# Kernel tuning notes

Hardware: AMD Instinct MI355X
Metric: run time of the kernel (lower is better)

The kernel has to match this reference:

```python
import jax, jax.numpy as jnp
import numpy as np
from jax import lax

DIM = 128; HEADS = 8; SPLIT = 4; MLP = 4
B = 8; H = 64; W = 64
EPS = 1e-5

def conv1x1(x, w, b):
    # x: (b,c,h,w), w: (o,c), b: (o,)
    return jnp.einsum('oc,bchw->bohw', w, x) + b[None, :, None, None]

def dwconv3(x, w, b):
    # depthwise 3x3, w: (C,1,3,3)
    c = x.shape[1]
    y = lax.conv_general_dilated(x, w, window_strides=(1, 1), padding=((1, 1), (1, 1)),
                                 feature_group_count=c,
                                 dimension_numbers=('NCHW', 'OIHW', 'NCHW'))
    return y + b[None, :, None, None]

def groupnorm1(x, g, bta):
    # GroupNorm with 1 group: normalize over (C,H,W) per sample
    mu = x.mean(axis=(1, 2, 3), keepdims=True)
    var = ((x - mu) ** 2).mean(axis=(1, 2, 3), keepdims=True)
    xn = (x - mu) * lax.rsqrt(var + EPS)
    return xn * g[None, :, None, None] + bta[None, :, None, None]

def eca(x, w):
    b, c, h, w_ = x.shape
    y = x.mean(axis=(2, 3))                         # (b,c)
    y = lax.conv_general_dilated(y[:, None, :], w, window_strides=(1,), padding=((2, 2),),
                                 dimension_numbers=('NCH', 'OIH', 'NCH'))  # (b,1,c)
    gate = jax.nn.sigmoid(y[:, 0])[:, :, None, None]
    return x * gate

def esa(x, alpha):
    x_se = x - x.mean(axis=(2, 3), keepdims=True)   # subtract per-channel GAP
    x_max = x_se.max(axis=1, keepdims=True)
    x_min = x_se.min(axis=1, keepdims=True)
    a = alpha[0]
    return x * jax.nn.sigmoid(x_max) * a + x * jax.nn.sigmoid(x_min) * (1.0 - a)

def eaa(q, k, v, h_sp, w_sp, cpe_w, cpe_b):
    b, c, h, w = q.shape
    hd = c // HEADS
    nh, nw = h // h_sp, w // w_sp
    L = h_sp * w_sp
    cpe = dwconv3(v, cpe_w, cpe_b)
    def win(t):
        t = t.reshape(b, c, nh, h_sp, nw, w_sp)
        t = t.transpose(0, 2, 4, 3, 5, 1).reshape(-1, L, HEADS, hd)
        return t.transpose(0, 2, 1, 3)  # (b*nh*nw, heads, L, hd)
    qw, kw, vw = win(q), win(k), win(v)
    attn = jax.nn.softmax(qw @ kw.transpose(0, 1, 3, 2), axis=-1)  # no scale, as in source
    o = attn @ vw                                    # (b*nh*nw, heads, L, hd)
    o = o.transpose(0, 2, 1, 3).reshape(b, nh, nw, h_sp, w_sp, c)
    o = o.transpose(0, 5, 1, 3, 2, 4).reshape(b, c, h, w)
    return o + cpe

def setup_inputs() -> dict:
    key = jax.random.key(0)
    ks = jax.random.split(key, 16)
    d = DIM
    z = lambda *s: jnp.zeros(s, jnp.float32)
    def n(i, shape, s=0.02):
        return jax.random.normal(ks[i], shape, dtype=jnp.float32) * s
    return dict(
        x=jax.random.normal(ks[0], (B, d, H, W), dtype=jnp.float32),
        eca_w=n(1, (1, 1, 5), 0.2),
        esa_alpha=jnp.ones((1,), jnp.float32),
        cpe1_w=n(2, (d, 1, 3, 3), 0.1), cpe1_b=z(d),
        g1=jnp.ones((d,), jnp.float32), b1=z(d),
        actp_w=n(3, (d, d)), actp_b=z(d),
        inp_w=n(4, (d, d)), inp_b=z(d),
        dwc_w=n(5, (d, 1, 3, 3), 0.1), dwc_b=z(d),
        qkv_w=n(6, (5 * d, d)), qkv_b=z(5 * d),
        eaax_w=n(7, (d, 1, 3, 3), 0.1), eaax_b=z(d),
        eaay_w=n(8, (d, 1, 3, 3), 0.1), eaay_b=z(d),
        outp_w=n(9, (d, d)), outp_b=z(d),
        cpe2_w=n(10, (d, 1, 3, 3), 0.1), cpe2_b=z(d),
        g2=jnp.ones((d,), jnp.float32), b2=z(d),
        mlp1_w=n(11, (MLP * d, d)), mlp1_b=z(MLP * d),
        mlp2_w=n(12, (d, MLP * d)), mlp2_b=z(d),
    )

def reference(x, eca_w, esa_alpha, cpe1_w, cpe1_b, g1, b1, actp_w, actp_b, inp_w, inp_b,
              dwc_w, dwc_b, qkv_w, qkv_b, eaax_w, eaax_b, eaay_w, eaay_b, outp_w, outp_b,
              cpe2_w, cpe2_b, g2, b2, mlp1_w, mlp1_b, mlp2_w, mlp2_b):
    b, c, h, w = x.shape
    x = eca(x, eca_w) + esa(x, esa_alpha)
    x = x + dwconv3(x, cpe1_w, cpe1_b)
    shortcut = x
    xn = groupnorm1(x, g1, b1)
    act_res = jax.nn.relu(conv1x1(xn, actp_w, actp_b))
    t = jax.nn.relu(dwconv3(conv1x1(xn, inp_w, inp_b), dwc_w, dwc_b))
    t = conv1x1(t, qkv_w, qkv_b)                     # (b, 5c, h, w)
    t5 = t.reshape(b, c, 5, h, w)                    # channel i::5 == t5[:,:,i]
    q0, k0, v0, q1, k1 = (t5[:, :, i] for i in range(5))
    a = eaa(q0, k0, v0, h, SPLIT, eaax_w, eaax_b) + eaa(q1, k1, v0, SPLIT, w, eaay_w, eaay_b)
    out = conv1x1(a * act_res, outp_w, outp_b) + shortcut
    out = out + dwconv3(out, cpe2_w, cpe2_b)
    mlp = conv1x1(jax.nn.relu(conv1x1(groupnorm1(out, g2, b2), mlp1_w, mlp1_b)), mlp2_w, mlp2_b)
    return mlp + out
```

## Files before the change

kernel.cpp:

```cpp
#include <hip/hip_runtime.h>

#define NPIX 4096
#define CDIM 128
#define BATCH 8
#define EPSN 1e-5f

typedef __attribute__((ext_vector_type(8))) short short8;
typedef __attribute__((ext_vector_type(4))) float f32x4;
typedef __attribute__((ext_vector_type(16))) float f32x16;

__device__ __forceinline__ float sigmoidf_(float x) { return 1.f / (1.f + __expf(-x)); }

__device__ __forceinline__ unsigned short f2b(float f) {
    unsigned int u = __float_as_uint(f);
    unsigned int r = (u + 0x7FFF + ((u >> 16) & 1)) >> 16;
    return (unsigned short)r;
}
__device__ __forceinline__ float b2f(unsigned short u) {
    return __uint_as_float((unsigned int)u << 16);
}

__device__ __forceinline__ int tok2pix(int mode, int wi, int l) {
    return (mode == 0) ? ((l >> 2) * 64 + wi * 4 + (l & 3))
                       : ((wi * 4 + (l >> 6)) * 64 + (l & 63));
}

__global__ __launch_bounds__(256) void convert_w_kernel(const float* __restrict__ qkv_w,
                                                        const float* __restrict__ mlp1_w,
                                                        const float* __restrict__ mlp2_w,
                                                        const float* __restrict__ actp_w,
                                                        const float* __restrict__ inp_w,
                                                        const float* __restrict__ outp_w,
                                                        const float* __restrict__ qkv_b,
                                                        const float* __restrict__ eaax_w,
                                                        const float* __restrict__ eaax_b,
                                                        const float* __restrict__ eaay_w,
                                                        const float* __restrict__ eaay_b,
                                                        const float* __restrict__ cpe1_w,
                                                        const float* __restrict__ dwc_w,
                                                        const float* __restrict__ cpe2_w,
                                                        unsigned short* __restrict__ dst,
                                                        float* __restrict__ qb_r,
                                                        float* __restrict__ wsT,
                                                        float* __restrict__ bsum,
                                                        float* __restrict__ cpe1T,
                                                        float* __restrict__ dwcT,
                                                        float* __restrict__ cpe2T) {
    int i = blockIdx.x * 256 + threadIdx.x;
    if (i >= 267520) return;
    if (i < 262144) {
        float v;
        if (i < 81920) {
            int o = i >> 7, c = i & 127;
            v = qkv_w[(size_t)(5 * (o & 127) + (o >> 7)) * 128 + c];
        } else if (i < 147456) v = mlp1_w[i - 81920];
        else if (i < 212992)   v = mlp2_w[i - 147456];
        else if (i < 229376)   v = actp_w[i - 212992];
        else if (i < 245760)   v = inp_w[i - 229376];
        else                   v = outp_w[i - 245760];
        dst[i] = f2b(v);
    } else {
        int j = i - 262144;
        if (j < 640) qb_r[j] = qkv_b[5 * (j & 127) + (j >> 7)];
        else if (j < 1792) {
            int idx = j - 640; int k = idx >> 7, c = idx & 127;
            wsT[idx] = eaax_w[c * 9 + k] + eaay_w[c * 9 + k];
        } else if (j < 1920) bsum[j - 1792] = eaax_b[j - 1792] + eaay_b[j - 1792];
        else if (j < 3072) {
            int idx = j - 1920; int k = idx >> 7, c = idx & 127;
            cpe1T[idx] = cpe1_w[c * 9 + k];
        } else if (j < 4224) {
            int idx = j - 3072; int k = idx >> 7, c = idx & 127;
            dwcT[idx] = dwc_w[c * 9 + k];
        } else {
            int idx = j - 4224; int k = idx >> 7, c = idx & 127;
            cpe2T[idx] = cpe2_w[c * 9 + k];
        }
    }
}

__global__ __launch_bounds__(256) void mean_bc_kernel(const float* __restrict__ x,
                                                      float* __restrict__ mean) {
    __shared__ float sb[4];
    int bc = blockIdx.x;
    const float* p = x + (size_t)bc * NPIX;
    float s = 0.f;
    for (int i = threadIdx.x; i < NPIX; i += 256) s += p[i];
#pragma unroll
    for (int off = 32; off > 0; off >>= 1) s += __shfl_down(s, off, 64);
    if ((threadIdx.x & 63) == 0) sb[threadIdx.x >> 6] = s;
    __syncthreads();
    if (threadIdx.x == 0) mean[bc] = (sb[0] + sb[1] + sb[2] + sb[3]) * (1.f / (float)NPIX);
}

__global__ void eca_gate_kernel(const float* __restrict__ mean, const float* __restrict__ w5,
                                float* __restrict__ gate) {
    int b = blockIdx.x, c = threadIdx.x;
    float s = 0.f;
#pragma unroll
    for (int k = 0; k < 5; ++k) {
        int cc = c + k - 2;
        if (cc >= 0 && cc < CDIM) s += w5[k] * mean[b * CDIM + cc];
    }
    gate[b * CDIM + c] = sigmoidf_(s);
}

__global__ __launch_bounds__(256) void esa_tr_kernel(const float* __restrict__ x,
                                                     const float* __restrict__ mean,
                                                     const float* __restrict__ gate,
                                                     const float* __restrict__ alpha_p,
                                                     float* __restrict__ y) {
    __shared__ float tile[128][65];
    __shared__ float smx[4][64], smn[4][64], ssc[64];
    int b = blockIdx.y, p0 = blockIdx.x * 64;
    int tx = threadIdx.x, pl = tx & 63, part = tx >> 6;
    const float* xb = x + (size_t)b * CDIM * NPIX;
    const float* mb = mean + b * CDIM;
    for (int c = part; c < CDIM; c += 4)
        tile[c][pl] = xb[(size_t)c * NPIX + p0 + pl];
    __syncthreads();
    float mx = -1e30f, mn = 1e30f;
#pragma unroll
    for (int cc = 0; cc < 32; ++cc) {
        int c = part * 32 + cc;
        float v = tile[c][pl] - mb[c];
        mx = fmaxf(mx, v); mn = fminf(mn, v);
    }
    smx[part][pl] = mx; smn[part][pl] = mn;
    __syncthreads();
    if (part == 0) {
        float m1 = fmaxf(fmaxf(smx[0][pl], smx[1][pl]), fmaxf(smx[2][pl], smx[3][pl]));
        float m2 = fminf(fminf(smn[0][pl], smn[1][pl]), fminf(smn[2][pl], smn[3][pl]));
        float a = alpha_p[0];
        ssc[pl] = sigmoidf_(m1) * a + sigmoidf_(m2) * (1.f - a);
    }
    __syncthreads();
    const float* gb = gate + b * CDIM;
    int c2 = tx & 127, pr = tx >> 7;
    float* yb = y + ((size_t)b * NPIX + p0) * CDIM;
    float gv = gb[c2];
    for (int p = pr; p < 64; p += 2)
        yb[(size_t)p * CDIM + c2] = tile[c2][p] * (gv + ssc[p]);
}

__global__ __launch_bounds__(256) void cpe_f32_kernel(const float* __restrict__ in,
                                                      const float* __restrict__ wT,
                                                      const float* __restrict__ bias,
                                                      float* __restrict__ out,
                                                      float* __restrict__ stats) {
    __shared__ float sb[8];
    int b = blockIdx.y, tx = threadIdx.x;
    int cg = tx & 15, pp = tx >> 4;
    int p = blockIdx.x * 16 + pp;
    int xx = p & 63, yy = p >> 6;
    int c0 = cg * 8;
    float acc[8], ctr[8];
#pragma unroll
    for (int j = 0; j < 8; ++j) acc[j] = bias[c0 + j];
#pragma unroll
    for (int dy = -1; dy <= 1; ++dy) {
        int y2 = yy + dy;
        if (y2 < 0 || y2 >= 64) continue;
#pragma unroll
        for (int dx = -1; dx <= 1; ++dx) {
            int x2 = xx + dx;
            if (x2 < 0 || x2 >= 64) continue;
            const float* ip = &in[((size_t)b * NPIX + y2 * 64 + x2) * 128 + c0];
            float4 v0 = *(const float4*)ip;
            float4 v1 = *(const float4*)(ip + 4);
            const float* wr = wT + ((dy + 1) * 3 + dx + 1) * 128 + c0;
            acc[0] += v0.x * wr[0]; acc[1] += v0.y * wr[1];
            acc[2] += v0.z * wr[2]; acc[3] += v0.w * wr[3];
            acc[4] += v1.x * wr[4]; acc[5] += v1.y * wr[5];
            acc[6] += v1.z * wr[6]; acc[7] += v1.w * wr[7];
            if (dy == 0 && dx == 0) {
                ctr[0] = v0.x; ctr[1] = v0.y; ctr[2] = v0.z; ctr[3] = v0.w;
                ctr[4] = v1.x; ctr[5] = v1.y; ctr[6] = v1.z; ctr[7] = v1.w;
            }
        }
    }
    float s = 0.f, s2 = 0.f;
    float r[8];
#pragma unroll
    for (int j = 0; j < 8; ++j) {
        r[j] = ctr[j] + acc[j];
        s += r[j]; s2 += r[j] * r[j];
    }
    float* op = &out[((size_t)b * NPIX + p) * 128 + c0];
    *(float4*)op = make_float4(r[0], r[1], r[2], r[3]);
    *(float4*)(op + 4) = make_float4(r[4], r[5], r[6], r[7]);
#pragma unroll
    for (int off = 32; off > 0; off >>= 1) {
        s += __shfl_down(s, off, 64);
        s2 += __shfl_down(s2, off, 64);
    }
    int wv = tx >> 6;
    if ((tx & 63) == 0) { sb[wv] = s; sb[4 + wv] = s2; }
    __syncthreads();
    if (tx == 0) {
        int slot = (b * 8 + (blockIdx.x & 7)) * 16;
        atomicAdd(&stats[slot], sb[0] + sb[1] + sb[2] + sb[3]);
        atomicAdd(&stats[slot + 1], sb[4] + sb[5] + sb[6] + sb[7]);
    }
}

__global__ __launch_bounds__(256) void gn_apply_kernel(const float* __restrict__ in,
                                                       const float* __restrict__ stats,
                                                       const float* __restrict__ g,
                                                       const float* __restrict__ bta,
                                                       unsigned short* __restrict__ dst) {
    int b = blockIdx.y;
    int i = blockIdx.x * 256 + threadIdx.x;
    float su = 0.f, sq = 0.f;
#pragma unroll
    for (int sl = 0; sl < 8; ++sl) {
        su += stats[(b * 8 + sl) * 16];
        sq += stats[(b * 8 + sl) * 16 + 1];
    }
    const float n = 1.f / (float)(CDIM * NPIX);
    float mu = su * n;
    float var = sq * n - mu * mu;
    float rr = rsqrtf(var + EPSN);
    int c0 = (i & 15) * 8;
    size_t idx = (size_t)b * (NPIX * 128) + (size_t)i * 8;
    float4 v0 = *(const float4*)&in[idx];
    float4 v1 = *(const float4*)&in[idx + 4];
    unsigned short o[8];
    o[0] = f2b((v0.x - mu) * rr * g[c0 + 0] + bta[c0 + 0]);
    o[1] = f2b((v0.y - mu) * rr * g[c0 + 1] + bta[c0 + 1]);
    o[2] = f2b((v0.z - mu) * rr * g[c0 + 2] + bta[c0 + 2]);
    o[3] = f2b((v0.w - mu) * rr * g[c0 + 3] + bta[c0 + 3]);
    o[4] = f2b((v1.x - mu) * rr * g[c0 + 4] + bta[c0 + 4]);
    o[5] = f2b((v1.y - mu) * rr * g[c0 + 5] + bta[c0 + 5]);
    o[6] = f2b((v1.z - mu) * rr * g[c0 + 6] + bta[c0 + 6]);
    o[7] = f2b((v1.w - mu) * rr * g[c0 + 7] + bta[c0 + 7]);
    *(uint4*)&dst[idx] = *(uint4*)o;
}

__global__ __launch_bounds__(256) void dwc_bf16_kernel(const unsigned short* __restrict__ in,
                                                       const float* __restrict__ wT,
                                                       const float* __restrict__ bias,
                                                       unsigned short* __restrict__ out) {
    int b = blockIdx.y, tx = threadIdx.x;
    int cg = tx & 15, pp = tx >> 4;
    int p = blockIdx.x * 16 + pp;
    int xx = p & 63, yy = p >> 6;
    int c0 = cg * 8;
    float acc[8];
#pragma unroll
    for (int j = 0; j < 8; ++j) acc[j] = bias[c0 + j];
#pragma unroll
    for (int dy = -1; dy <= 1; ++dy) {
        int y2 = yy + dy;
        if (y2 < 0 || y2 >= 64) continue;
#pragma unroll
        for (int dx = -1; dx <= 1; ++dx) {
            int x2 = xx + dx;
            if (x2 < 0 || x2 >= 64) continue;
            unsigned short v[8];
            *(uint4*)v = *(const uint4*)&in[((size_t)b * NPIX + y2 * 64 + x2) * 128 + c0];
            const float* wr = wT + ((dy + 1) * 3 + dx + 1) * 128 + c0;
#pragma unroll
            for (int j = 0; j < 8; ++j) acc[j] += b2f(v[j]) * wr[j];
        }
    }
    unsigned short o[8];
#pragma unroll
    for (int j = 0; j < 8; ++j) o[j] = f2b(fmaxf(acc[j], 0.f));
    *(uint4*)&out[((size_t)b * NPIX + p) * 128 + c0] = *(uint4*)o;
}

__global__ __launch_bounds__(256) void conv_mfma_kernel(const unsigned short* __restrict__ in_t,
                                                        const unsigned short* __restrict__ w,
                                                        const float* __restrict__ bias,
                                                        const float* __restrict__ res,
                                                        float* __restrict__ out,
                                                        unsigned short* __restrict__ out_t,
                                                        int Cin, int Cout, int relu, int nchw) {
    __shared__ __align__(16) unsigned short A_s[128][136];
    __shared__ __align__(16) unsigned short B_s[128][136];
    int b = blockIdx.z, p0 = blockIdx.x * 128, o0 = blockIdx.y * 128;
    int tx = threadIdx.x;
    int wave = tx >> 6, lane = tx & 63;
    int wm = wave & 1, wn = wave >> 1;
    int quad = lane >> 4, l16 = lane & 15;

    f32x4 acc[4][4];
#pragma unroll
    for (int mt = 0; mt < 4; ++mt) {
#pragma unroll
        for (int r = 0; r < 4; ++r) {
            float bv = bias[o0 + wm * 64 + mt * 16 + quad * 4 + r];
#pragma unroll
            for (int nt = 0; nt < 4; ++nt) acc[mt][nt][r] = bv;
        }
    }

    for (int k0 = 0; k0 < Cin; k0 += 128) {
#pragma unroll
        for (int j = 0; j < 8; ++j) {
            int idx = tx + 256 * j;
            int row = idx >> 4, c16 = idx & 15;
            *(uint4*)&A_s[row][c16 * 8] =
                *(const uint4*)&w[(size_t)(o0 + row) * Cin + k0 + c16 * 8];
            *(uint4*)&B_s[row][c16 * 8] =
                *(const uint4*)&in_t[((size_t)b * NPIX + p0 + row) * Cin + k0 + c16 * 8];
        }
        __syncthreads();
#pragma unroll
        for (int ks = 0; ks < 128; ks += 32) {
            short8 af[4], bf[4];
#pragma unroll
            for (int mt = 0; mt < 4; ++mt)
                af[mt] = *(const short8*)&A_s[wm * 64 + mt * 16 + l16][ks + quad * 8];
#pragma unroll
            for (int nt = 0; nt < 4; ++nt)
                bf[nt] = *(const short8*)&B_s[wn * 64 + nt * 16 + l16][ks + quad * 8];
#pragma unroll
            for (int mt = 0; mt < 4; ++mt)
#pragma unroll
                for (int nt = 0; nt < 4; ++nt)
                    acc[mt][nt] = __builtin_amdgcn_mfma_f32_16x16x32_bf16(
                        af[mt], bf[nt], acc[mt][nt], 0, 0, 0);
        }
        __syncthreads();
    }

    if (out_t) {
#pragma unroll
        for (int mt = 0; mt < 4; ++mt) {
#pragma unroll
            for (int nt = 0; nt < 4; ++nt) {
                int p = p0 + wn * 64 + nt * 16 + l16;
                int ob = o0 + wm * 64 + mt * 16 + quad * 4;
                ushort4 u;
                float v0 = acc[mt][nt][0], v1 = acc[mt][nt][1];
                float v2 = acc[mt][nt][2], v3 = acc[mt][nt][3];
                if (relu) { v0 = fmaxf(v0, 0.f); v1 = fmaxf(v1, 0.f);
                            v2 = fmaxf(v2, 0.f); v3 = fmaxf(v3, 0.f); }
                u.x = f2b(v0); u.y = f2b(v1); u.z = f2b(v2); u.w = f2b(v3);
                *(ushort4*)&out_t[((size_t)b * NPIX + p) * Cout + ob] = u;
            }
        }
    } else if (!nchw) {
#pragma unroll
        for (int mt = 0; mt < 4; ++mt) {
#pragma unroll
            for (int nt = 0; nt < 4; ++nt) {
                int p = p0 + wn * 64 + nt * 16 + l16;
                int ob = o0 + wm * 64 + mt * 16 + quad * 4;
                size_t ix = ((size_t)b * NPIX + p) * Cout + ob;
                float4 v = make_float4(acc[mt][nt][0], acc[mt][nt][1],
                                       acc[mt][nt][2], acc[mt][nt][3]);
                if (relu) { v.x = fmaxf(v.x, 0.f); v.y = fmaxf(v.y, 0.f);
                            v.z = fmaxf(v.z, 0.f); v.w = fmaxf(v.w, 0.f); }
                if (res) {
                    float4 rv = *(const float4*)&res[ix];
                    v.x += rv.x; v.y += rv.y; v.z += rv.z; v.w += rv.w;
                }
                *(float4*)&out[ix] = v;
            }
        }
    } else {
        float* outb = out + (size_t)b * Cout * NPIX;
#pragma unroll
        for (int mt = 0; mt < 4; ++mt) {
#pragma unroll
            for (int nt = 0; nt < 4; ++nt) {
                int p = p0 + wn * 64 + nt * 16 + l16;
                int ob = o0 + wm * 64 + mt * 16 + quad * 4;
                float4 rv = make_float4(0.f, 0.f, 0.f, 0.f);
                if (res) rv = *(const float4*)&res[((size_t)b * NPIX + p) * 128 + ob];
#pragma unroll
                for (int r = 0; r < 4; ++r) {
                    float v = acc[mt][nt][r];
                    if (relu) v = fmaxf(v, 0.f);
                    v += (r == 0 ? rv.x : r == 1 ? rv.y : r == 2 ? rv.z : rv.w);
                    outb[(size_t)(ob + r) * NPIX + p] = v;
                }
            }
        }
    }
}

__global__ __launch_bounds__(256) void attn_dual_kernel(const unsigned short* __restrict__ t_t,
                                                        float* __restrict__ a0,
                                                        float* __restrict__ a1) {
    __shared__ __align__(16) unsigned short Vt[16][264];
    int wi = blockIdx.x, head = blockIdx.y;
    int z = blockIdx.z;
    int b = z >> 1, which = z & 1;
    int qoff = which ? 384 : 0;
    int koff = which ? 512 : 128;
    int mode = which;
    float* a_out = which ? a1 : a0;
    int tx = threadIdx.x;
    int wave = tx >> 6, l = tx & 63;
    int l32 = l & 31, half = l >> 5;
    const size_t base = (size_t)b * NPIX;
    const int hc = head * 16;

    {
        int p = tok2pix(mode, wi, tx);
        const unsigned short* vp = &t_t[(base + p) * 640 + 256 + hc];
        unsigned short tmp[16];
        *(uint4*)&tmp[0] = *(const uint4*)vp;
        *(uint4*)&tmp[8] = *(const uint4*)(vp + 8);
#pragma unroll
        for (int d = 0; d < 16; ++d) Vt[d][tx] = tmp[d];
    }
    __syncthreads();

    for (int qi = 0; qi < 2; ++qi) {
        int qs = qi * 4 + wave;
        int qp = tok2pix(mode, wi, qs * 32 + l32);
        short8 qf = *(const short8*)&t_t[(base + qp) * 640 + qoff + hc + half * 8];
        f32x16 o_acc;
#pragma unroll
        for (int r = 0; r < 16; ++r) o_acc[r] = 0.f;
        float rs = 0.f;
#pragma unroll
        for (int nt = 0; nt < 8; ++nt) {
            int kp = tok2pix(mode, wi, nt * 32 + l32);
            short8 kf = *(const short8*)&t_t[(base + kp) * 640 + koff + hc + half * 8];
            f32x16 zz;
#pragma unroll
            for (int r = 0; r < 16; ++r) zz[r] = 0.f;
            f32x16 s = __builtin_amdgcn_mfma_f32_32x32x16_bf16(kf, qf, zz, 0, 0, 0);
            unsigned int pk[8];
#pragma unroll
            for (int i = 0; i < 8; ++i) {
                float e0 = __expf(s[2 * i]);
                float e1 = __expf(s[2 * i + 1]);
                rs += e0 + e1;
                pk[i] = __builtin_amdgcn_perm(__float_as_uint(e1), __float_as_uint(e0),
                                              0x07060302u);
            }
            unsigned int xpk[8];
#pragma unroll
            for (int i = 0; i < 8; ++i)
                xpk[i] = (unsigned int)__shfl_xor((int)pk[i], 32, 64);
            unsigned int u0[4], u1[4];
            if (half == 0) {
                u0[0] = pk[0]; u0[1] = pk[1]; u0[2] = xpk[0]; u0[3] = xpk[1];
                u1[0] = pk[4]; u1[1] = pk[5]; u1[2] = xpk[4]; u1[3] = xpk[5];
            } else {
                u0[0] = xpk[2]; u0[1] = xpk[3]; u0[2] = pk[2]; u0[3] = pk[3];
                u1[0] = xpk[6]; u1[1] = xpk[7]; u1[2] = pk[6]; u1[3] = pk[7];
            }
            short8 vf0, vf1;
#pragma unroll
            for (int r = 0; r < 8; ++r) { vf0[r] = 0; vf1[r] = 0; }
            if (l32 < 16) {
                vf0 = *(const short8*)&Vt[l32][nt * 32 + half * 8];
                vf1 = *(const short8*)&Vt[l32][nt * 32 + 16 + half * 8];
            }
            o_acc = __builtin_amdgcn_mfma_f32_32x32x16_bf16(vf0, *(short8*)u0, o_acc, 0, 0, 0);
            o_acc = __builtin_amdgcn_mfma_f32_32x32x16_bf16(vf1, *(short8*)u1, o_acc, 0, 0, 0);
        }
        rs += __shfl_xor(rs, 32, 64);
        float rinv = 1.f / rs;
        float* dst = a_out + (base + qp) * 128 + hc;
#pragma unroll
        for (int r = 0; r < 8; ++r) {
            int d = (r & 3) + 8 * (r >> 2) + 4 * half;
            dst[d] = o_acc[r] * rinv;
        }
    }
}

__global__ __launch_bounds__(256) void cpe_nhwc_kernel(const unsigned short* __restrict__ t_t,
                                                       const float* __restrict__ wT,
                                                       const float* __restrict__ bsum,
                                                       float* __restrict__ a_out) {
    int b = blockIdx.y;
    int tx = threadIdx.x;
    int cg = tx & 15, pp = tx >> 4;
    int p = blockIdx.x * 16 + pp;
    int xx = p & 63, yy = p >> 6;
    int c0 = cg * 8;
    float acc[8];
#pragma unroll
    for (int j = 0; j < 8; ++j) acc[j] = bsum[c0 + j];
#pragma unroll
    for (int dy = -1; dy <= 1; ++dy) {
        int y2 = yy + dy;
        if (y2 < 0 || y2 >= 64) continue;
#pragma unroll
        for (int dx = -1; dx <= 1; ++dx) {
            int x2 = xx + dx;
            if (x2 < 0 || x2 >= 64) continue;
            int pn = y2 * 64 + x2;
            unsigned short v[8];
            *(uint4*)v = *(const uint4*)&t_t[((size_t)b * NPIX + pn) * 640 + 256 + c0];
            const float* wr = wT + ((dy + 1) * 3 + dx + 1) * 128 + c0;
#pragma unroll
            for (int j = 0; j < 8; ++j) acc[j] += b2f(v[j]) * wr[j];
        }
    }
    float* dst = a_out + ((size_t)b * NPIX + p) * 128 + c0;
#pragma unroll
    for (int j = 0; j < 8; ++j) dst[j] += acc[j];
}

__global__ __launch_bounds__(256) void mul3_kernel(const float* __restrict__ a0,
                                                   const float* __restrict__ a1,
                                                   const unsigned short* __restrict__ act,
                                                   unsigned short* __restrict__ dst) {
    size_t i = ((size_t)blockIdx.x * 256 + threadIdx.x) * 8;
    float4 x0 = *(const float4*)&a0[i];
    float4 x1 = *(const float4*)&a0[i + 4];
    float4 y0 = *(const float4*)&a1[i];
    float4 y1 = *(const float4*)&a1[i + 4];
    unsigned short t[8];
    *(uint4*)t = *(const uint4*)&act[i];
    unsigned short r[8];
    r[0] = f2b((x0.x + y0.x) * b2f(t[0])); r[1] = f2b((x0.y + y0.y) * b2f(t[1]));
    r[2] = f2b((x0.z + y0.z) * b2f(t[2])); r[3] = f2b((x0.w + y0.w) * b2f(t[3]));
    r[4] = f2b((x1.x + y1.x) * b2f(t[4])); r[5] = f2b((x1.y + y1.y) * b2f(t[5]));
    r[6] = f2b((x1.z + y1.z) * b2f(t[6])); r[7] = f2b((x1.w + y1.w) * b2f(t[7]));
    *(uint4*)&dst[i] = *(uint4*)r;
}

extern "C" void kernel_launch(void* const* d_in, const int* in_sizes, int n_in,
                              void* d_out, int out_size, void* d_ws, size_t ws_size,
                              hipStream_t stream) {
    const float* x       = (const float*)d_in[0];
    const float* eca_w   = (const float*)d_in[1];
    const float* esa_al  = (const float*)d_in[2];
    const float* cpe1_w  = (const float*)d_in[3];  const float* cpe1_b = (const float*)d_in[4];
    const float* g1      = (const float*)d_in[5];  const float* b1     = (const float*)d_in[6];
    const float* actp_w  = (const float*)d_in[7];  const float* actp_b = (const float*)d_in[8];
    const float* inp_w   = (const float*)d_in[9];  const float* inp_b  = (const float*)d_in[10];
    const float* dwc_w   = (const float*)d_in[11]; const float* dwc_b  = (const float*)d_in[12];
    const float* qkv_w   = (const float*)d_in[13]; const float* qkv_b  = (const float*)d_in[14];
    const float* eaax_w  = (const float*)d_in[15]; const float* eaax_b = (const float*)d_in[16];
    const float* eaay_w  = (const float*)d_in[17]; const float* eaay_b = (const float*)d_in[18];
    const float* outp_w  = (const float*)d_in[19]; const float* outp_b = (const float*)d_in[20];
    const float* cpe2_w  = (const float*)d_in[21]; const float* cpe2_b = (const float*)d_in[22];
    const float* g2      = (const float*)d_in[23]; const float* b2     = (const float*)d_in[24];
    const float* mlp1_w  = (const float*)d_in[25]; const float* mlp1_b = (const float*)d_in[26];
    const float* mlp2_w  = (const float*)d_in[27]; const float* mlp2_b = (const float*)d_in[28];

    float* ws = (float*)d_ws;
    unsigned short* U = (unsigned short*)d_ws;
    const size_t E = (size_t)BATCH * CDIM * NPIX;

    float* y_nhwc  = ws;
    float* a0      = ws;
    float* sc_nhwc = ws + E;
    unsigned short* xn_t  = U + 4 * E;
    unsigned short* act_t = U + 5 * E;
    unsigned short* it_t  = U + 6 * E;
    unsigned short* tin_t = U + 7 * E;
    float* a1      = ws + 4 * E;
    unsigned short* t_t   = U + 10 * E;
    unsigned short* m_t   = U + 15 * E;
    float* out_nhwc = ws + 8 * E;
    float* out2    = ws + 2 * E;
    unsigned short* g2_t  = U + 6 * E;
    unsigned short* hid_t = U + 10 * E;
    unsigned short* wpool = U + 20 * E;
    unsigned short* wq  = wpool;
    unsigned short* wm1 = wpool + 81920;
    unsigned short* wm2 = wpool + 147456;
    unsigned short* wa  = wpool + 212992;
    unsigned short* wi_ = wpool + 229376;
    unsigned short* wo  = wpool + 245760;
    float* fb     = ws + 10 * E + 131072;
    float* meanb  = fb;
    float* gateb  = fb + 1024;
    float* gstats = fb + 2048;
    float* qb_r   = fb + 4096;
    float* wsT    = fb + 4736;
    float* bsum   = fb + 5888;
    float* cpe1T  = fb + 6016;
    float* dwcT   = fb + 7168;
    float* cpe2T  = fb + 8320;

    hipMemsetAsync(gstats, 0, 2048 * sizeof(float), stream);
    convert_w_kernel<<<1045, 256, 0, stream>>>(qkv_w, mlp1_w, mlp2_w, actp_w, inp_w, outp_w,
                                               qkv_b, eaax_w, eaax_b, eaay_w, eaay_b,
                                               cpe1_w, dwc_w, cpe2_w,
                                               wpool, qb_r, wsT, bsum, cpe1T, dwcT, cpe2T);

    mean_bc_kernel<<<BATCH * CDIM, 256, 0, stream>>>(x, meanb);
    eca_gate_kernel<<<BATCH, CDIM, 0, stream>>>(meanb, eca_w, gateb);
    esa_tr_kernel<<<dim3(64, BATCH), 256, 0, stream>>>(x, meanb, gateb, esa_al, y_nhwc);
    cpe_f32_kernel<<<dim3(256, BATCH), 256, 0, stream>>>(y_nhwc, cpe1T, cpe1_b, sc_nhwc, gstats);
    gn_apply_kernel<<<dim3(256, BATCH), 256, 0, stream>>>(sc_nhwc, gstats, g1, b1, xn_t);
    conv_mfma_kernel<<<dim3(32, 1, BATCH), 256, 0, stream>>>(xn_t, wa, actp_b, nullptr, nullptr,
                                                             act_t, 128, 128, 1, 0);
    conv_mfma_kernel<<<dim3(32, 1, BATCH), 256, 0, stream>>>(xn_t, wi_, inp_b, nullptr, nullptr,
                                                             it_t, 128, 128, 0, 0);
    dwc_bf16_kernel<<<dim3(256, BATCH), 256, 0, stream>>>(it_t, dwcT, dwc_b, tin_t);
    conv_mfma_kernel<<<dim3(32, 5, BATCH), 256, 0, stream>>>(tin_t, wq, qb_r, nullptr, nullptr,
                                                             t_t, 128, 640, 0, 0);
    attn_dual_kernel<<<dim3(16, 8, 2 * BATCH), 256, 0, stream>>>(t_t, a0, a1);
    cpe_nhwc_kernel<<<dim3(256, BATCH), 256, 0, stream>>>(t_t, wsT, bsum, a1);
    mul3_kernel<<<2048, 256, 0, stream>>>(a0, a1, act_t, m_t);
    conv_mfma_kernel<<<dim3(32, 1, BATCH), 256, 0, stream>>>(m_t, wo, outp_b, sc_nhwc, out_nhwc,
                                                             nullptr, 128, 128, 0, 0);
    cpe_f32_kernel<<<dim3(256, BATCH), 256, 0, stream>>>(out_nhwc, cpe2T, cpe2_b, out2,
                                                         gstats + 1024);
    gn_apply_kernel<<<dim3(256, BATCH), 256, 0, stream>>>(out2, gstats + 1024, g2, b2, g2_t);
    conv_mfma_kernel<<<dim3(32, 4, BATCH), 256, 0, stream>>>(g2_t, wm1, mlp1_b, nullptr, nullptr,
                                                             hid_t, 128, 512, 1, 0);
    conv_mfma_kernel<<<dim3(32, 1, BATCH), 256, 0, stream>>>(hid_t, wm2, mlp2_b, out2,
                                                             (float*)d_out, nullptr, 512, 128, 0, 1);
}
```

Measured before the change: 329.4 us.

## Fuse groupnorm into conv GEMM loads, merge act/in convs, fold eca and cpe kernels

GroupNorm application now happens inside the MFMA conv's B-tile load from fp32, which removes the separate normalize pass and its bf16 intermediate. The actp and inp 1x1 convs share one launch, with relu applied only to the first output block. The ECA gate is computed inside the ESA kernel, and the attention CPE is fused with the mul3 kernel. The GEMM pixel tile shrinks from 128 to 64 to raise block count, at the cost of reloading weights more often and redoing the normalize work for each output tile.

New measurement: 314.0 us. -4.7%, faster.

```diff
diff --git a/kernel.cpp b/kernel.cpp
--- a/kernel.cpp
+++ b/kernel.cpp
@@ -39,15 +39,18 @@
                                                         const float* __restrict__ cpe1_w,
                                                         const float* __restrict__ dwc_w,
                                                         const float* __restrict__ cpe2_w,
+                                                        const float* __restrict__ actp_b,
+                                                        const float* __restrict__ inp_b,
                                                         unsigned short* __restrict__ dst,
                                                         float* __restrict__ qb_r,
                                                         float* __restrict__ wsT,
                                                         float* __restrict__ bsum,
                                                         float* __restrict__ cpe1T,
                                                         float* __restrict__ dwcT,
-                                                        float* __restrict__ cpe2T) {
+                                                        float* __restrict__ cpe2T,
+                                                        float* __restrict__ abi) {
     int i = blockIdx.x * 256 + threadIdx.x;
-    if (i >= 267520) return;
+    if (i >= 267776) return;
     if (i < 262144) {
         float v;
         if (i < 81920) {
@@ -72,9 +75,12 @@
         } else if (j < 4224) {
             int idx = j - 3072; int k = idx >> 7, c = idx & 127;
             dwcT[idx] = dwc_w[c * 9 + k];
-        } else {
+        } else if (j < 5376) {
             int idx = j - 4224; int k = idx >> 7, c = idx & 127;
             cpe2T[idx] = cpe2_w[c * 9 + k];
+        } else {
+            int idx = j - 5376;
+            abi[idx] = (idx < 128) ? actp_b[idx] : inp_b[idx - 128];
         }
     }
 }
@@ -93,25 +99,13 @@
     if (threadIdx.x == 0) mean[bc] = (sb[0] + sb[1] + sb[2] + sb[3]) * (1.f / (float)NPIX);
 }
 
-__global__ void eca_gate_kernel(const float* __restrict__ mean, const float* __restrict__ w5,
-                                float* __restrict__ gate) {
-    int b = blockIdx.x, c = threadIdx.x;
-    float s = 0.f;
-#pragma unroll
-    for (int k = 0; k < 5; ++k) {
-        int cc = c + k - 2;
-        if (cc >= 0 && cc < CDIM) s += w5[k] * mean[b * CDIM + cc];
-    }
-    gate[b * CDIM + c] = sigmoidf_(s);
-}
-
 __global__ __launch_bounds__(256) void esa_tr_kernel(const float* __restrict__ x,
                                                      const float* __restrict__ mean,
-                                                     const float* __restrict__ gate,
+                                                     const float* __restrict__ w5,
                                                      const float* __restrict__ alpha_p,
                                                      float* __restrict__ y) {
     __shared__ float tile[128][65];
-    __shared__ float smx[4][64], smn[4][64], ssc[64];
+    __shared__ float smx[4][64], smn[4][64], ssc[64], gat[128];
     int b = blockIdx.y, p0 = blockIdx.x * 64;
     int tx = threadIdx.x, pl = tx & 63, part = tx >> 6;
     const float* xb = x + (size_t)b * CDIM * NPIX;
@@ -128,6 +122,15 @@
     }
     smx[part][pl] = mx; smn[part][pl] = mn;
     __syncthreads();
+    if (tx < 128) {
+        float s = 0.f;
+#pragma unroll
+        for (int k = 0; k < 5; ++k) {
+            int cc = tx + k - 2;
+            if (cc >= 0 && cc < CDIM) s += w5[k] * mb[cc];
+        }
+        gat[tx] = sigmoidf_(s);
+    }
     if (part == 0) {
         float m1 = fmaxf(fmaxf(smx[0][pl], smx[1][pl]), fmaxf(smx[2][pl], smx[3][pl]));
         float m2 = fminf(fminf(smn[0][pl], smn[1][pl]), fminf(smn[2][pl], smn[3][pl]));
@@ -135,10 +138,9 @@
         ssc[pl] = sigmoidf_(m1) * a + sigmoidf_(m2) * (1.f - a);
     }
     __syncthreads();
-    const float* gb = gate + b * CDIM;
     int c2 = tx & 127, pr = tx >> 7;
     float* yb = y + ((size_t)b * NPIX + p0) * CDIM;
-    float gv = gb[c2];
+    float gv = gat[c2];
     for (int p = pr; p < 64; p += 2)
         yb[(size_t)p * CDIM + c2] = tile[c2][p] * (gv + ssc[p]);
 }
@@ -204,39 +206,6 @@
     }
 }
 
-__global__ __launch_bounds__(256) void gn_apply_kernel(const float* __restrict__ in,
-                                                       const float* __restrict__ stats,
-                                                       const float* __restrict__ g,
-                                                       const float* __restrict__ bta,
-                                                       unsigned short* __restrict__ dst) {
-    int b = blockIdx.y;
-    int i = blockIdx.x * 256 + threadIdx.x;
-    float su = 0.f, sq = 0.f;
-#pragma unroll
-    for (int sl = 0; sl < 8; ++sl) {
-        su += stats[(b * 8 + sl) * 16];
-        sq += stats[(b * 8 + sl) * 16 + 1];
-    }
-    const float n = 1.f / (float)(CDIM * NPIX);
-    float mu = su * n;
-    float var = sq * n - mu * mu;
-    float rr = rsqrtf(var + EPSN);
-    int c0 = (i & 15) * 8;
-    size_t idx = (size_t)b * (NPIX * 128) + (size_t)i * 8;
-    float4 v0 = *(const float4*)&in[idx];
-    float4 v1 = *(const float4*)&in[idx + 4];
-    unsigned short o[8];
-    o[0] = f2b((v0.x - mu) * rr * g[c0 + 0] + bta[c0 + 0]);
-    o[1] = f2b((v0.y - mu) * rr * g[c0 + 1] + bta[c0 + 1]);
-    o[2] = f2b((v0.z - mu) * rr * g[c0 + 2] + bta[c0 + 2]);
-    o[3] = f2b((v0.w - mu) * rr * g[c0 + 3] + bta[c0 + 3]);
-    o[4] = f2b((v1.x - mu) * rr * g[c0 + 4] + bta[c0 + 4]);
-    o[5] = f2b((v1.y - mu) * rr * g[c0 + 5] + bta[c0 + 5]);
-    o[6] = f2b((v1.z - mu) * rr * g[c0 + 6] + bta[c0 + 6]);
-    o[7] = f2b((v1.w - mu) * rr * g[c0 + 7] + bta[c0 + 7]);
-    *(uint4*)&dst[idx] = *(uint4*)o;
-}
-
 __global__ __launch_bounds__(256) void dwc_bf16_kernel(const unsigned short* __restrict__ in,
                                                        const float* __restrict__ wT,
                                                        const float* __restrict__ bias,
@@ -271,28 +240,47 @@
 }
 
 __global__ __launch_bounds__(256) void conv_mfma_kernel(const unsigned short* __restrict__ in_t,
+                                                        const float* __restrict__ in_f32,
+                                                        const float* __restrict__ gst,
+                                                        const float* __restrict__ gg,
+                                                        const float* __restrict__ gbta,
                                                         const unsigned short* __restrict__ w,
                                                         const float* __restrict__ bias,
                                                         const float* __restrict__ res,
                                                         float* __restrict__ out,
                                                         unsigned short* __restrict__ out_t,
+                                                        unsigned short* __restrict__ out_t2,
                                                         int Cin, int Cout, int relu, int nchw) {
     __shared__ __align__(16) unsigned short A_s[128][136];
-    __shared__ __align__(16) unsigned short B_s[128][136];
-    int b = blockIdx.z, p0 = blockIdx.x * 128, o0 = blockIdx.y * 128;
+    __shared__ __align__(16) unsigned short B_s[64][136];
+    int b = blockIdx.z, p0 = blockIdx.x * 64, o0 = blockIdx.y * 128;
     int tx = threadIdx.x;
     int wave = tx >> 6, lane = tx & 63;
     int wm = wave & 1, wn = wave >> 1;
     int quad = lane >> 4, l16 = lane & 15;
 
-    f32x4 acc[4][4];
+    float mu = 0.f, rr = 1.f;
+    if (in_f32) {
+        float su = 0.f, sq = 0.f;
+#pragma unroll
+        for (int sl = 0; sl < 8; ++sl) {
+            su += gst[(b * 8 + sl) * 16];
+            sq += gst[(b * 8 + sl) * 16 + 1];
+        }
+        const float n = 1.f / (float)(CDIM * NPIX);
+        mu = su * n;
+        float var = sq * n - mu * mu;
+        rr = rsqrtf(var + EPSN);
+    }
+
+    f32x4 acc[4][2];
 #pragma unroll
     for (int mt = 0; mt < 4; ++mt) {
 #pragma unroll
         for (int r = 0; r < 4; ++r) {
             float bv = bias[o0 + wm * 64 + mt * 16 + quad * 4 + r];
 #pragma unroll
-            for (int nt = 0; nt < 4; ++nt) acc[mt][nt][r] = bv;
+            for (int nt = 0; nt < 2; ++nt) acc[mt][nt][r] = bv;
         }
     }
 
@@ -303,57 +291,88 @@
             int row = idx >> 4, c16 = idx & 15;
             *(uint4*)&A_s[row][c16 * 8] =
                 *(const uint4*)&w[(size_t)(o0 + row) * Cin + k0 + c16 * 8];
-            *(uint4*)&B_s[row][c16 * 8] =
-                *(const uint4*)&in_t[((size_t)b * NPIX + p0 + row) * Cin + k0 + c16 * 8];
+        }
+        if (in_f32) {
+#pragma unroll
+            for (int j = 0; j < 4; ++j) {
+                int idx = tx + 256 * j;
+                int row = idx >> 4, c16 = idx & 15;
+                int ch = c16 * 8;
+                const float* ip = &in_f32[((size_t)b * NPIX + p0 + row) * 128 + ch];
+                float4 v0 = *(const float4*)ip;
+                float4 v1 = *(const float4*)(ip + 4);
+                unsigned short o[8];
+                o[0] = f2b((v0.x - mu) * rr * gg[ch + 0] + gbta[ch + 0]);
+                o[1] = f2b((v0.y - mu) * rr * gg[ch + 1] + gbta[ch + 1]);
+                o[2] = f2b((v0.z - mu) * rr * gg[ch + 2] + gbta[ch + 2]);
+                o[3] = f2b((v0.w - mu) * rr * gg[ch + 3] + gbta[ch + 3]);
+                o[4] = f2b((v1.x - mu) * rr * gg[ch + 4] + gbta[ch + 4]);
+                o[5] = f2b((v1.y - mu) * rr * gg[ch + 5] + gbta[ch + 5]);
+                o[6] = f2b((v1.z - mu) * rr * gg[ch + 6] + gbta[ch + 6]);
+                o[7] = f2b((v1.w - mu) * rr * gg[ch + 7] + gbta[ch + 7]);
+                *(uint4*)&B_s[row][c16 * 8] = *(uint4*)o;
+            }
+        } else {
+#pragma unroll
+            for (int j = 0; j < 4; ++j) {
+                int idx = tx + 256 * j;
+                int row = idx >> 4, c16 = idx & 15;
+                *(uint4*)&B_s[row][c16 * 8] =
+                    *(const uint4*)&in_t[((size_t)b * NPIX + p0 + row) * Cin + k0 + c16 * 8];
+            }
         }
         __syncthreads();
 #pragma unroll
         for (int ks = 0; ks < 128; ks += 32) {
-            short8 af[4], bf[4];
+            short8 af[4], bf[2];
 #pragma unroll
             for (int mt = 0; mt < 4; ++mt)
                 af[mt] = *(const short8*)&A_s[wm * 64 + mt * 16 + l16][ks + quad * 8];
 #pragma unroll
-            for (int nt = 0; nt < 4; ++nt)
-                bf[nt] = *(const short8*)&B_s[wn * 64 + nt * 16 + l16][ks + quad * 8];
+            for (int nt = 0; nt < 2; ++nt)
+                bf[nt] = *(const short8*)&B_s[wn * 32 + nt * 16 + l16][ks + quad * 8];
 #pragma unroll
             for (int mt = 0; mt < 4; ++mt)
 #pragma unroll
-                for (int nt = 0; nt < 4; ++nt)
+                for (int nt = 0; nt < 2; ++nt)
                     acc[mt][nt] = __builtin_amdgcn_mfma_f32_16x16x32_bf16(
                         af[mt], bf[nt], acc[mt][nt], 0, 0, 0);
         }
         __syncthreads();
     }
 
+    int dorelu = (relu == 1) || (relu == 2 && blockIdx.y == 0);
     if (out_t) {
 #pragma unroll
         for (int mt = 0; mt < 4; ++mt) {
 #pragma unroll
-            for (int nt = 0; nt < 4; ++nt) {
-                int p = p0 + wn * 64 + nt * 16 + l16;
+            for (int nt = 0; nt < 2; ++nt) {
+                int p = p0 + wn * 32 + nt * 16 + l16;
                 int ob = o0 + wm * 64 + mt * 16 + quad * 4;
+                unsigned short* dbuf = out_t;
+                int oc = ob;
+                if (out_t2 && o0 >= 128) { dbuf = out_t2; oc = ob - 128; }
                 ushort4 u;
                 float v0 = acc[mt][nt][0], v1 = acc[mt][nt][1];
                 float v2 = acc[mt][nt][2], v3 = acc[mt][nt][3];
-                if (relu) { v0 = fmaxf(v0, 0.f); v1 = fmaxf(v1, 0.f);
-                            v2 = fmaxf(v2, 0.f); v3 = fmaxf(v3, 0.f); }
+                if (dorelu) { v0 = fmaxf(v0, 0.f); v1 = fmaxf(v1, 0.f);
+                              v2 = fmaxf(v2, 0.f); v3 = fmaxf(v3, 0.f); }
                 u.x = f2b(v0); u.y = f2b(v1); u.z = f2b(v2); u.w = f2b(v3);
-                *(ushort4*)&out_t[((size_t)b * NPIX + p) * Cout + ob] = u;
+                *(ushort4*)&dbuf[((size_t)b * NPIX + p) * Cout + oc] = u;
             }
         }
     } else if (!nchw) {
 #pragma unroll
         for (int mt = 0; mt < 4; ++mt) {
 #pragma unroll
-            for (int nt = 0; nt < 4; ++nt) {
-                int p = p0 + wn * 64 + nt * 16 + l16;
+            for (int nt = 0; nt < 2; ++nt) {
+                int p = p0 + wn * 32 + nt * 16 + l16;
                 int ob = o0 + wm * 64 + mt * 16 + quad * 4;
                 size_t ix = ((size_t)b * NPIX + p) * Cout + ob;
                 float4 v = make_float4(acc[mt][nt][0], acc[mt][nt][1],
                                        acc[mt][nt][2], acc[mt][nt][3]);
-                if (relu) { v.x = fmaxf(v.x, 0.f); v.y = fmaxf(v.y, 0.f);
-                            v.z = fmaxf(v.z, 0.f); v.w = fmaxf(v.w, 0.f); }
+                if (dorelu) { v.x = fmaxf(v.x, 0.f); v.y = fmaxf(v.y, 0.f);
+                              v.z = fmaxf(v.z, 0.f); v.w = fmaxf(v.w, 0.f); }
                 if (res) {
                     float4 rv = *(const float4*)&res[ix];
                     v.x += rv.x; v.y += rv.y; v.z += rv.z; v.w += rv.w;
@@ -366,15 +385,15 @@
 #pragma unroll
         for (int mt = 0; mt < 4; ++mt) {
 #pragma unroll
-            for (int nt = 0; nt < 4; ++nt) {
-                int p = p0 + wn * 64 + nt * 16 + l16;
+            for (int nt = 0; nt < 2; ++nt) {
+                int p = p0 + wn * 32 + nt * 16 + l16;
                 int ob = o0 + wm * 64 + mt * 16 + quad * 4;
                 float4 rv = make_float4(0.f, 0.f, 0.f, 0.f);
                 if (res) rv = *(const float4*)&res[((size_t)b * NPIX + p) * 128 + ob];
 #pragma unroll
                 for (int r = 0; r < 4; ++r) {
                     float v = acc[mt][nt][r];
-                    if (relu) v = fmaxf(v, 0.f);
+                    if (dorelu) v = fmaxf(v, 0.f);
                     v += (r == 0 ? rv.x : r == 1 ? rv.y : r == 2 ? rv.z : rv.w);
                     outb[(size_t)(ob + r) * NPIX + p] = v;
                 }
@@ -469,10 +488,13 @@
     }
 }
 
-__global__ __launch_bounds__(256) void cpe_nhwc_kernel(const unsigned short* __restrict__ t_t,
+__global__ __launch_bounds__(256) void mul3_cpe_kernel(const float* __restrict__ a0,
+                                                       const float* __restrict__ a1,
+                                                       const unsigned short* __restrict__ act,
+                                                       const unsigned short* __restrict__ t_t,
                                                        const float* __restrict__ wT,
                                                        const float* __restrict__ bsum,
-                                                       float* __restrict__ a_out) {
+                                                       unsigned short* __restrict__ dst) {
     int b = blockIdx.y;
     int tx = threadIdx.x;
     int cg = tx & 15, pp = tx >> 4;
@@ -498,28 +520,23 @@
             for (int j = 0; j < 8; ++j) acc[j] += b2f(v[j]) * wr[j];
         }
     }
-    float* dst = a_out + ((size_t)b * NPIX + p) * 128 + c0;
-#pragma unroll
-    for (int j = 0; j < 8; ++j) dst[j] += acc[j];
-}
-
-__global__ __launch_bounds__(256) void mul3_kernel(const float* __restrict__ a0,
-                                                   const float* __restrict__ a1,
-                                                   const unsigned short* __restrict__ act,
-                                                   unsigned short* __restrict__ dst) {
-    size_t i = ((size_t)blockIdx.x * 256 + threadIdx.x) * 8;
-    float4 x0 = *(const float4*)&a0[i];
-    float4 x1 = *(const float4*)&a0[i + 4];
-    float4 y0 = *(const float4*)&a1[i];
-    float4 y1 = *(const float4*)&a1[i + 4];
+    size_t base = ((size_t)b * NPIX + p) * 128 + c0;
+    float4 x0 = *(const float4*)&a0[base];
+    float4 x1 = *(const float4*)&a0[base + 4];
+    float4 y0 = *(const float4*)&a1[base];
+    float4 y1 = *(const float4*)&a1[base + 4];
     unsigned short t[8];
-    *(uint4*)t = *(const uint4*)&act[i];
+    *(uint4*)t = *(const uint4*)&act[base];
     unsigned short r[8];
-    r[0] = f2b((x0.x + y0.x) * b2f(t[0])); r[1] = f2b((x0.y + y0.y) * b2f(t[1]));
-    r[2] = f2b((x0.z + y0.z) * b2f(t[2])); r[3] = f2b((x0.w + y0.w) * b2f(t[3]));
-    r[4] = f2b((x1.x + y1.x) * b2f(t[4])); r[5] = f2b((x1.y + y1.y) * b2f(t[5]));
-    r[6] = f2b((x1.z + y1.z) * b2f(t[6])); r[7] = f2b((x1.w + y1.w) * b2f(t[7]));
-    *(uint4*)&dst[i] = *(uint4*)r;
+    r[0] = f2b((x0.x + y0.x + acc[0]) * b2f(t[0]));
+    r[1] = f2b((x0.y + y0.y + acc[1]) * b2f(t[1]));
+    r[2] = f2b((x0.z + y0.z + acc[2]) * b2f(t[2]));
+    r[3] = f2b((x0.w + y0.w + acc[3]) * b2f(t[3]));
+    r[4] = f2b((x1.x + y1.x + acc[4]) * b2f(t[4]));
+    r[5] = f2b((x1.y + y1.y + acc[5]) * b2f(t[5]));
+    r[6] = f2b((x1.z + y1.z + acc[6]) * b2f(t[6]));
+    r[7] = f2b((x1.w + y1.w + acc[7]) * b2f(t[7]));
+    *(uint4*)&dst[base] = *(uint4*)r;
 }
 
 extern "C" void kernel_launch(void* const* d_in, const int* in_sizes, int n_in,
@@ -549,7 +566,6 @@
     float* y_nhwc  = ws;
     float* a0      = ws;
     float* sc_nhwc = ws + E;
-    unsigned short* xn_t  = U + 4 * E;
     unsigned short* act_t = U + 5 * E;
     unsigned short* it_t  = U + 6 * E;
     unsigned short* tin_t = U + 7 * E;
@@ -558,18 +574,15 @@
     unsigned short* m_t   = U + 15 * E;
     float* out_nhwc = ws + 8 * E;
     float* out2    = ws + 2 * E;
-    unsigned short* g2_t  = U + 6 * E;
     unsigned short* hid_t = U + 10 * E;
     unsigned short* wpool = U + 20 * E;
     unsigned short* wq  = wpool;
     unsigned short* wm1 = wpool + 81920;
     unsigned short* wm2 = wpool + 147456;
-    unsigned short* wa  = wpool + 212992;
-    unsigned short* wi_ = wpool + 229376;
+    unsigned short* wai = wpool + 212992;
     unsigned short* wo  = wpool + 245760;
     float* fb     = ws + 10 * E + 131072;
     float* meanb  = fb;
-    float* gateb  = fb + 1024;
     float* gstats = fb + 2048;
     float* qb_r   = fb + 4096;
     float* wsT    = fb + 4736;
@@ -577,35 +590,37 @@
     float* cpe1T  = fb + 6016;
     float* dwcT   = fb + 7168;
     float* cpe2T  = fb + 8320;
+    float* abi    = fb + 9472;
 
     hipMemsetAsync(gstats, 0, 2048 * sizeof(float), stream);
-    convert_w_kernel<<<1045, 256, 0, stream>>>(qkv_w, mlp1_w, mlp2_w, actp_w, inp_w, outp_w,
+    convert_w_kernel<<<1046, 256, 0, stream>>>(qkv_w, mlp1_w, mlp2_w, actp_w, inp_w, outp_w,
                                                qkv_b, eaax_w, eaax_b, eaay_w, eaay_b,
-                                               cpe1_w, dwc_w, cpe2_w,
-                                               wpool, qb_r, wsT, bsum, cpe1T, dwcT, cpe2T);
+                                               cpe1_w, dwc_w, cpe2_w, actp_b, inp_b,
+                                               wpool, qb_r, wsT, bsum, cpe1T, dwcT, cpe2T, abi);
 
     mean_bc_kernel<<<BATCH * CDIM, 256, 0, stream>>>(x, meanb);
-    eca_gate_kernel<<<BATCH, CDIM, 0, stream>>>(meanb, eca_w, gateb);
-    esa_tr_kernel<<<dim3(64, BATCH), 256, 0, stream>>>(x, meanb, gateb, esa_al, y_nhwc);
+    esa_tr_kernel<<<dim3(64, BATCH), 256, 0, stream>>>(x, meanb, eca_w, esa_al, y_nhwc);
     cpe_f32_kernel<<<dim3(256, BATCH), 256, 0, stream>>>(y_nhwc, cpe1T, cpe1_b, sc_nhwc, gstats);
-    gn_apply_kernel<<<dim3(256, BATCH), 256, 0, stream>>>(sc_nhwc, gstats, g1, b1, xn_t);
-    conv_mfma_kernel<<<dim3(32, 1, BATCH), 256, 0, stream>>>(xn_t, wa, actp_b, nullptr, nullptr,
-                                                             act_t, 128, 128, 1, 0);
-    conv_mfma_kernel<<<dim3(32, 1, BATCH), 256, 0, stream>>>(xn_t, wi_, inp_b, nullptr, nullptr,
-                                                             it_t, 128, 128, 0, 0);
+    conv_mfma_kernel<<<dim3(64, 2, BATCH), 256, 0, stream>>>(nullptr, sc_nhwc, gstats, g1, b1,
+                                                             wai, abi, nullptr, nullptr,
+                                                             act_t, it_t, 128, 128, 2, 0);
     dwc_bf16_kernel<<<dim3(256, BATCH), 256, 0, stream>>>(it_t, dwcT, dwc_b, tin_t);
-    conv_mfma_kernel<<<dim3(32, 5, BATCH), 256, 0, stream>>>(tin_t, wq, qb_r, nullptr, nullptr,
-                                                             t_t, 128, 640, 0, 0);
+    conv_mfma_kernel<<<dim3(64, 5, BATCH), 256, 0, stream>>>(tin_t, nullptr, nullptr, nullptr,
+                                                             nullptr, wq, qb_r, nullptr, nullptr,
+                                                             t_t, nullptr, 128, 640, 0, 0);
     attn_dual_kernel<<<dim3(16, 8, 2 * BATCH), 256, 0, stream>>>(t_t, a0, a1);
-    cpe_nhwc_kernel<<<dim3(256, BATCH), 256, 0, stream>>>(t_t, wsT, bsum, a1);
-    mul3_kernel<<<2048, 256, 0, stream>>>(a0, a1, act_t, m_t);
-    conv_mfma_kernel<<<dim3(32, 1, BATCH), 256, 0, stream>>>(m_t, wo, outp_b, sc_nhwc, out_nhwc,
-                                                             nullptr, 128, 128, 0, 0);
+    mul3_cpe_kernel<<<dim3(256, BATCH), 256, 0, stream>>>(a0, a1, act_t, t_t, wsT, bsum, m_t);
+    conv_mfma_kernel<<<dim3(64, 1, BATCH), 256, 0, stream>>>(m_t, nullptr, nullptr, nullptr,
+                                                             nullptr, wo, outp_b, sc_nhwc,
+                                                             out_nhwc, nullptr, nullptr,
+                                                             128, 128, 0, 0);
     cpe_f32_kernel<<<dim3(256, BATCH), 256, 0, stream>>>(out_nhwc, cpe2T, cpe2_b, out2,
                                                          gstats + 1024);
-    gn_apply_kernel<<<dim3(256, BATCH), 256, 0, stream>>>(out2, gstats + 1024, g2, b2, g2_t);
-    conv_mfma_kernel<<<dim3(32, 4, BATCH), 256, 0, stream>>>(g2_t, wm1, mlp1_b, nullptr, nullptr,
-                                                             hid_t, 128, 512, 1, 0);
-    conv_mfma_kernel<<<dim3(32, 1, BATCH), 256, 0, stream>>>(hid_t, wm2, mlp2_b, out2,
-                                                             (float*)d_out, nullptr, 512, 128, 0, 1);
-}
+    conv_mfma_kernel<<<dim3(64, 4, BATCH), 256, 0, stream>>>(nullptr, out2, gstats + 1024, g2, b2,
+                                                             wm1, mlp1_b, nullptr, nullptr,
+                                                             hid_t, nullptr, 128, 512, 1, 0);
+    conv_mfma_kernel<<<dim3(64, 1, BATCH), 256, 0, stream>>>(hid_t, nullptr, nullptr, nullptr,
+                                                             nullptr, wm2, mlp2_b, out2,
+                                                             (float*)d_out, nullptr, nullptr,
+                                                             512, 128, 0, 1);
+}
```
